# Performance work log

Measured on AMD Instinct MI355X. Metric: run time of the kernel, lower is better.

## Reference

```python
import jax, jax.numpy as jnp
import numpy as np

N_E = 8192      # codebook size
E_DIM = 256     # codebook dim
BETA = 0.25

def setup_inputs() -> dict:
    key = jax.random.key(0)
    k1, k2 = jax.random.split(key)
    z = jax.random.normal(k1, (4, E_DIM, 16, 16, 16), dtype=jnp.float32)
    weight = jax.random.normal(k2, (N_E, E_DIM), dtype=jnp.float32)
    return {"z": z, "weight": weight}

def reference(z, weight):
    # b c d h w -> b d h w c
    z_t = jnp.transpose(z, (0, 2, 3, 4, 1))
    zf = z_t.reshape(-1, E_DIM)                          # [N, e_dim]
    # l2 pairwise distances: |z|^2 + |w|^2 - 2 z.w^T
    d = (jnp.sum(zf * zf, axis=1, keepdims=True)
         + jnp.sum(weight * weight, axis=1)
         - 2.0 * jnp.einsum('bd,nd->bn', zf, weight))    # [N, n_e]
    idx = jnp.argmin(d, axis=1)                          # [N]
    z_q = weight[idx].reshape(z_t.shape)                 # gather lookup
    # perplexity from cluster assignment histogram (avoids dense one-hot)
    counts = jax.ops.segment_sum(jnp.ones_like(idx, dtype=z.dtype), idx,
                                 num_segments=N_E)
    avg_probs = counts / zf.shape[0]
    perplexity = jnp.exp(-jnp.sum(avg_probs * jnp.log(avg_probs + 1e-10)))
    # commitment loss (z_q detached)
    loss = BETA * jnp.mean((jax.lax.stop_gradient(z_q) - z_t) ** 2)
    # straight-through estimator
    z_q_st = z_t + jax.lax.stop_gradient(z_q - z_t)
    out = jnp.transpose(z_q_st, (0, 4, 1, 2, 3))         # b d h w c -> b c d h w
    return out, loss, perplexity, idx
```

## Files before the change

kernel.cpp:

```cpp
#include <hip/hip_runtime.h>
#include <stdint.h>


#define M_TOTAL 16384
#define N_CODES 8192
#define KDIM    256
#define SPATIAL 4096
#define NSPLIT  8
#define CODES_PER_SPLIT  1024
#define CHUNK_CODES      32
#define CHUNKS_PER_SPLIT 32
#define CHUNK_HALFS      8192
#define CHUNK_BYTES      16384

typedef _Float16 v8hf __attribute__((ext_vector_type(8)));
typedef _Float16 v4hf __attribute__((ext_vector_type(4)));
typedef float    v4f  __attribute__((ext_vector_type(4)));

__global__ __launch_bounds__(256) void prep_kernel(
    const float* __restrict__ w, const float* __restrict__ z,
    _Float16* __restrict__ wpk, float* __restrict__ hw_arr,
    _Float16* __restrict__ zfrag,
    int* __restrict__ counts, double* __restrict__ loss_acc,
    int* __restrict__ done_ctr)
{
    const int bid = blockIdx.x;
    const int t = threadIdx.x;
    if (bid < 2048) {
        const int n = bid * 4 + (t >> 6);
        const int lane = t & 63;
        v4f v = ((const v4f*)(w + (size_t)n * KDIM))[lane];
        v4hf hv;
        float s = 0.0f;
#pragma unroll
        for (int j = 0; j < 4; j++) {
            float f = v[j];
            s += f * f;
            hv[j] = (_Float16)f;
        }
        const int chunk = n >> 5;
        const int row   = n & 31;
        const int gg    = (lane >> 1) ^ (n & 7);
        size_t off = (size_t)chunk * CHUNK_HALFS + row * 256 + gg * 8 + (lane & 1) * 4;
        *(v4hf*)(wpk + off) = hv;
#pragma unroll
        for (int o = 32; o >= 1; o >>= 1) s += __shfl_xor(s, o);
        if (lane == 0) hw_arr[n] = 1024.0f - 0.5f * s;
        const int gi = bid * 4 + (t >> 6);
        if (t < 4 && false) {}
        const int ci = bid * 4 + (t & 3);
        if ((t >> 2) == 0) counts[ci] = 0;
        if (bid == 0 && t == 0) { *loss_acc = 0.0; *done_ctr = 0; }
        (void)gi;
    } else {
        const int g16  = (bid - 2048) * 4 + (t >> 6);
        const int lane = t & 63;
        const int r    = lane & 15;
        const int q    = lane >> 4;
        const int row  = g16 * 16 + r;
        const int b    = row >> 12;
        const int s    = row & (SPATIAL - 1);
        const float* zb = z + ((size_t)b << 20) + s;
#pragma unroll
        for (int ks = 0; ks < 8; ks++) {
            v8hf o;
#pragma unroll
            for (int j = 0; j < 8; j++)
                o[j] = (_Float16)zb[(size_t)(ks * 32 + q * 8 + j) << 12];
            *(v8hf*)(zfrag + ((size_t)(g16 * 8 + ks) * 64 + lane) * 8) = o;
        }
    }
}

__device__ __forceinline__ void top2max_merge(uint32_t& v1, int& i1, uint32_t& v2, int& i2,
                                              uint32_t o1, int oi1, uint32_t o2, int oi2) {
    bool ob = (o1 > v1) || (o1 == v1 && oi1 < i1);
    uint32_t n1v, n2v; int n1i, n2i;
    if (ob) {
        bool t2 = (v1 > o2) || (v1 == o2 && i1 < oi2);
        n1v = o1; n1i = oi1;
        n2v = t2 ? v1 : o2; n2i = t2 ? i1 : oi2;
    } else {
        bool t2 = (o1 > v2) || (o1 == v2 && oi1 < i2);
        n1v = v1; n1i = i1;
        n2v = t2 ? o1 : v2; n2i = t2 ? oi1 : i2;
    }
    v1 = n1v; i1 = n1i; v2 = n2v; i2 = n2i;
}

__global__ __launch_bounds__(256, 4) void gemm_kernel(
    const _Float16* __restrict__ zfrag,
    const _Float16* __restrict__ wpk,
    const float* __restrict__ hw_arr,
    int4* __restrict__ candbuf)
{
    __shared__ __align__(16) _Float16 lds[2][CHUNK_HALFS];
    __shared__ float hw_lds[CODES_PER_SPLIT];

    const int bid   = blockIdx.x;
    const int split = bid & 7;
    const int rb    = bid >> 3;
    const int i0    = rb * 128;
    const int tid   = threadIdx.x;
    const int wave  = tid >> 6;
    const int lane  = tid & 63;
    const int r     = lane & 15;
    const int q     = lane >> 4;

    const char* wsplit = (const char*)wpk + (size_t)split * (CODES_PER_SPLIT * KDIM * 2);
    auto stage = [&](int chunk, int buf) {
        const char* gb = wsplit + (size_t)chunk * CHUNK_BYTES + tid * 16;
        _Float16* lb = &lds[buf][tid * 8];
#pragma unroll
        for (int j = 0; j < 4; j++) {
            __builtin_amdgcn_global_load_lds(
                (const __attribute__((address_space(1))) void*)(gb + j * 4096),
                (__attribute__((address_space(3))) void*)(lb + j * 2048), 16, 0, 0);
        }
    };
    stage(0, 0);

    {
        v4f h = *(const v4f*)(hw_arr + split * CODES_PER_SPLIT + tid * 4);
        *(v4f*)&hw_lds[tid * 4] = h;
    }

    v8hf a[2][8];
    {
        const int g16 = (i0 + wave * 32) >> 4;
#pragma unroll
        for (int mt = 0; mt < 2; mt++) {
#pragma unroll
            for (int ks = 0; ks < 8; ks++)
                a[mt][ks] = *(const v8hf*)(zfrag +
                    ((size_t)((g16 + mt) * 8 + ks) * 64 + lane) * 8);
        }
    }

    uint32_t k1[2][4], k2[2][4];
#pragma unroll
    for (int mt = 0; mt < 2; mt++)
#pragma unroll
    for (int g = 0; g < 4; g++) { k1[mt][g] = 0u; k2[mt][g] = 0u; }

    const int swz = r & 7;

    __syncthreads();

#pragma unroll 1
    for (int it = 0; it < CHUNKS_PER_SPLIT; it++) {
        const int buf = it & 1;
        if (it + 1 < CHUNKS_PER_SPLIT) stage(it + 1, buf ^ 1);

        const float hw0 = hw_lds[it * 32 + r];
        const float hw1 = hw_lds[it * 32 + 16 + r];
        v4f acc[2][2];
#pragma unroll
        for (int mt = 0; mt < 2; mt++) {
            acc[mt][0] = (v4f){hw0, hw0, hw0, hw0};
            acc[mt][1] = (v4f){hw1, hw1, hw1, hw1};
        }
        const _Float16* L = &lds[buf][0];
#pragma unroll
        for (int st = 0; st < 2; st++) {
            const int rowoff = (st * 16 + r) * 256;
#pragma unroll
            for (int ks = 0; ks < 8; ks++) {
                const int gran = ((ks << 2) | q) ^ swz;
                v8hf bh = *(const v8hf*)(L + rowoff + (gran << 3));
#pragma unroll
                for (int mt = 0; mt < 2; mt++)
                    acc[mt][st] = __builtin_amdgcn_mfma_f32_16x16x32_f16(a[mt][ks], bh, acc[mt][st], 0, 0, 0);
            }
        }
#pragma unroll
        for (int st = 0; st < 2; st++) {
            const uint32_t tag = (uint32_t)(it * 2 + st);
#pragma unroll
            for (int mt = 0; mt < 2; mt++)
#pragma unroll
            for (int g = 0; g < 4; g++) {
                uint32_t key = (__float_as_uint(acc[mt][st][g]) & 0xFFFFFFC0u) | tag;
                uint32_t o1 = k1[mt][g], o2 = k2[mt][g];
                uint32_t hi = key > o2 ? key : o2;
                k2[mt][g] = hi < o1 ? hi : o1;
                k1[mt][g] = key > o1 ? key : o1;
            }
        }
        __syncthreads();
    }

    const int nsbase = split * CODES_PER_SPLIT + r;
#pragma unroll
    for (int mt = 0; mt < 2; mt++) {
#pragma unroll
        for (int g = 0; g < 4; g++) {
            uint32_t K1 = k1[mt][g], K2 = k2[mt][g];
            int n1 = nsbase + (int)((K1 & 63u) << 4);
            int n2 = nsbase + (int)((K2 & 63u) << 4);
#pragma unroll
            for (int off = 1; off < 16; off <<= 1) {
                uint32_t o1 = __shfl_xor(K1, off);
                int     on1 = __shfl_xor(n1, off);
                uint32_t o2 = __shfl_xor(K2, off);
                int     on2 = __shfl_xor(n2, off);
                top2max_merge(K1, n1, K2, n2, o1, on1, o2, on2);
            }
            if (r == 0) {
                const int row = i0 + wave * 32 + mt * 16 + q * 4 + g;
                candbuf[(size_t)row * 8 + split] = make_int4((int)K1, n1, (int)K2, n2);
            }
        }
    }
}

__global__ __launch_bounds__(256) void finish_kernel(
    const float* __restrict__ z, const float* __restrict__ weight,
    const int4* __restrict__ candbuf,
    int* __restrict__ counts, double* __restrict__ loss_acc,
    int* __restrict__ done_ctr,
    float* __restrict__ out, float* __restrict__ out_scalars,
    float* __restrict__ out_idx_f)
{
    __shared__ int4  s_cand[32][8];
    __shared__ float s_zw[32][KDIM + 1];
    __shared__ int   s_fi[32];
    __shared__ double s_red[4];
    __shared__ int   s_last;

    const int i0 = blockIdx.x * 32;
    const int b  = i0 >> 12;
    const int s0 = i0 & (SPATIAL - 1);
    const int t  = threadIdx.x;

    s_cand[t >> 3][t & 7] = candbuf[(size_t)(i0 + (t >> 3)) * 8 + (t & 7)];

    for (int e = t; e < 32 * KDIM; e += 256) {
        const int c = e >> 5, rr = e & 31;
        s_zw[rr][c] = z[((size_t)b << 20) + ((size_t)c << 12) + s0 + rr];
    }
    __syncthreads();

    const int row = t >> 3, seg = t & 7;
    float zs[32];
#pragma unroll
    for (int j = 0; j < 32; j++) zs[j] = s_zw[row][seg * 32 + j];

    float da[16];
    float dmin_a = 3.4e38f;
#pragma unroll
    for (int sp = 0; sp < 8; sp++) {
        int4 c = s_cand[row][sp];
        da[sp * 2]     = 2048.0f - 2.0f * __uint_as_float((uint32_t)c.x & 0xFFFFFFC0u);
        da[sp * 2 + 1] = 2048.0f - 2.0f * __uint_as_float((uint32_t)c.z & 0xFFFFFFC0u);
        dmin_a = fminf(dmin_a, fminf(da[sp * 2], da[sp * 2 + 1]));
    }
    const float cutoff = dmin_a + 0.5f;

    double dbest = 1e300; int nbest = 0x7fffffff;
#pragma unroll 1
    for (int c = 0; c < 16; c++) {
        if (da[c] > cutoff) continue;
        int4 cc = s_cand[row][c >> 1];
        const int n = (c & 1) ? cc.w : cc.y;
        const float* wr = weight + (size_t)n * KDIM + seg * 32;
        double d = 0.0;
#pragma unroll
        for (int j = 0; j < 32; j++) {
            double df = (double)zs[j] - (double)wr[j];
            d += df * df;
        }
#pragma unroll
        for (int o = 1; o < 8; o <<= 1) d += __shfl_xor(d, o);
        if (d < dbest || (d == dbest && n < nbest)) { dbest = d; nbest = n; }
    }

    double lsum = 0.0;
    if (seg == 0) {
        s_fi[row] = nbest;
        out_idx_f[i0 + row] = (float)nbest;
        atomicAdd(&counts[nbest], 1);
        lsum = dbest;
    }
#pragma unroll
    for (int o = 1; o < 64; o <<= 1) lsum += __shfl_xor(lsum, o);
    if ((t & 63) == 0) s_red[t >> 6] = lsum;
    __syncthreads();
    if (t == 0) atomicAdd(loss_acc, s_red[0] + s_red[1] + s_red[2] + s_red[3]);

    for (int e = t; e < 32 * KDIM; e += 256) {
        const int rr = e >> 8, c = e & 255;
        s_zw[rr][c] = weight[(size_t)s_fi[rr] * KDIM + c];
    }
    __syncthreads();
    const int m = t & 31, c0 = t >> 5;
    const size_t obase = ((size_t)b << 20) + (size_t)(s0 + m);
    for (int c = c0; c < KDIM; c += 8)
        out[obase + ((size_t)c << 12)] = s_zw[m][c];

    if (t == 0) {
        __threadfence();
        int old = __hip_atomic_fetch_add(done_ctr, 1, __ATOMIC_ACQ_REL,
                                         __HIP_MEMORY_SCOPE_AGENT);
        s_last = (old == (int)gridDim.x - 1);
    }
    __syncthreads();
    if (s_last) {
        double s = 0.0;
        for (int n = t; n < N_CODES; n += 256) {
            int c = __hip_atomic_load(&counts[n], __ATOMIC_RELAXED,
                                      __HIP_MEMORY_SCOPE_AGENT);
            double p = (double)c / (double)M_TOTAL;
            s -= p * log(p + 1e-10);
        }
#pragma unroll
        for (int o = 32; o >= 1; o >>= 1) s += __shfl_xor(s, o);
        if ((t & 63) == 0) s_red[t >> 6] = s;
        __syncthreads();
        if (t == 0) {
            double tot = s_red[0] + s_red[1] + s_red[2] + s_red[3];
            double l = __hip_atomic_load(loss_acc, __ATOMIC_RELAXED,
                                         __HIP_MEMORY_SCOPE_AGENT);
            out_scalars[0] = (float)(0.25 * l / (double)(M_TOTAL * KDIM));
            out_scalars[1] = (float)exp(tot);
        }
    }
}

extern "C" void kernel_launch(void* const* d_in, const int* in_sizes, int n_in,
                              void* d_out, int out_size, void* d_ws, size_t ws_size,
                              hipStream_t stream) {
    const float* z      = (const float*)d_in[0];
    const float* weight = (const float*)d_in[1];
    float* out = (float*)d_out;

    size_t off = 0;
    auto carve = [&](size_t bytes) {
        void* p = (char*)d_ws + off;
        off += (bytes + 255) & ~(size_t)255;
        return p;
    };
    _Float16* wpk     = (_Float16*)carve((size_t)N_CODES * KDIM * 2);
    float*    hw_arr  = (float*)   carve((size_t)N_CODES * 4);
    _Float16* zfrag   = (_Float16*)carve((size_t)M_TOTAL * KDIM * 2);
    int4*     candbuf = (int4*)    carve((size_t)M_TOTAL * 8 * 16);
    int*      counts  = (int*)     carve((size_t)N_CODES * 4);
    double*   lossac  = (double*)  carve(16);
    int*      donec   = (int*)     carve(16);

    float* out_scalars = out + (size_t)4 * KDIM * SPATIAL;
    float* out_idx_f   = out_scalars + 2;

    prep_kernel<<<dim3(2048 + 256), dim3(256), 0, stream>>>(
        weight, z, wpk, hw_arr, zfrag, counts, lossac, donec);
    gemm_kernel<<<dim3(128 * NSPLIT), dim3(256), 0, stream>>>(
        zfrag, wpk, hw_arr, candbuf);
    finish_kernel<<<dim3(M_TOTAL / 32), dim3(256), 0, stream>>>(
        z, weight, candbuf, counts, lossac, donec, out, out_scalars, out_idx_f);
}
```

Measured before the change: 219.8 us.

## Fuse prep, GEMM and finish kernels into one persistent kernel with grid barriers

Merges the three launches into a single 1024-block kernel whose phases are separated by software grid barriers (atomic counter plus spin-wait), with the barrier counters cleared by a memset. The z transpose to fp16 fragments now goes through an LDS tile for coalesced writes, and the finish phase handles 16 rows per block instead of 32. This removes two kernel launch gaps and tail effects. The risks are deadlock if all 1024 blocks are not co-resident, an added memset launch, and spin-wait overhead.

```diff
diff --git a/kernel.cpp b/kernel.cpp
--- a/kernel.cpp
+++ b/kernel.cpp
@@ -8,69 +8,14 @@
 #define SPATIAL 4096
 #define NSPLIT  8
 #define CODES_PER_SPLIT  1024
-#define CHUNK_CODES      32
 #define CHUNKS_PER_SPLIT 32
 #define CHUNK_HALFS      8192
 #define CHUNK_BYTES      16384
+#define GRID_BLOCKS      1024
 
 typedef _Float16 v8hf __attribute__((ext_vector_type(8)));
 typedef _Float16 v4hf __attribute__((ext_vector_type(4)));
 typedef float    v4f  __attribute__((ext_vector_type(4)));
-
-__global__ __launch_bounds__(256) void prep_kernel(
-    const float* __restrict__ w, const float* __restrict__ z,
-    _Float16* __restrict__ wpk, float* __restrict__ hw_arr,
-    _Float16* __restrict__ zfrag,
-    int* __restrict__ counts, double* __restrict__ loss_acc,
-    int* __restrict__ done_ctr)
-{
-    const int bid = blockIdx.x;
-    const int t = threadIdx.x;
-    if (bid < 2048) {
-        const int n = bid * 4 + (t >> 6);
-        const int lane = t & 63;
-        v4f v = ((const v4f*)(w + (size_t)n * KDIM))[lane];
-        v4hf hv;
-        float s = 0.0f;
-#pragma unroll
-        for (int j = 0; j < 4; j++) {
-            float f = v[j];
-            s += f * f;
-            hv[j] = (_Float16)f;
-        }
-        const int chunk = n >> 5;
-        const int row   = n & 31;
-        const int gg    = (lane >> 1) ^ (n & 7);
-        size_t off = (size_t)chunk * CHUNK_HALFS + row * 256 + gg * 8 + (lane & 1) * 4;
-        *(v4hf*)(wpk + off) = hv;
-#pragma unroll
-        for (int o = 32; o >= 1; o >>= 1) s += __shfl_xor(s, o);
-        if (lane == 0) hw_arr[n] = 1024.0f - 0.5f * s;
-        const int gi = bid * 4 + (t >> 6);
-        if (t < 4 && false) {}
-        const int ci = bid * 4 + (t & 3);
-        if ((t >> 2) == 0) counts[ci] = 0;
-        if (bid == 0 && t == 0) { *loss_acc = 0.0; *done_ctr = 0; }
-        (void)gi;
-    } else {
-        const int g16  = (bid - 2048) * 4 + (t >> 6);
-        const int lane = t & 63;
-        const int r    = lane & 15;
-        const int q    = lane >> 4;
-        const int row  = g16 * 16 + r;
-        const int b    = row >> 12;
-        const int s    = row & (SPATIAL - 1);
-        const float* zb = z + ((size_t)b << 20) + s;
-#pragma unroll
-        for (int ks = 0; ks < 8; ks++) {
-            v8hf o;
-#pragma unroll
-            for (int j = 0; j < 8; j++)
-                o[j] = (_Float16)zb[(size_t)(ks * 32 + q * 8 + j) << 12];
-            *(v8hf*)(zfrag + ((size_t)(g16 * 8 + ks) * 64 + lane) * 8) = o;
-        }
-    }
-}
 
 __device__ __forceinline__ void top2max_merge(uint32_t& v1, int& i1, uint32_t& v2, int& i2,
                                               uint32_t o1, int oi1, uint32_t o2, int oi2) {
@@ -88,241 +33,309 @@
     v1 = n1v; i1 = n1i; v2 = n2v; i2 = n2i;
 }
 
-__global__ __launch_bounds__(256, 4) void gemm_kernel(
-    const _Float16* __restrict__ zfrag,
-    const _Float16* __restrict__ wpk,
-    const float* __restrict__ hw_arr,
-    int4* __restrict__ candbuf)
-{
-    __shared__ __align__(16) _Float16 lds[2][CHUNK_HALFS];
-    __shared__ float hw_lds[CODES_PER_SPLIT];
-
-    const int bid   = blockIdx.x;
-    const int split = bid & 7;
-    const int rb    = bid >> 3;
-    const int i0    = rb * 128;
-    const int tid   = threadIdx.x;
-    const int wave  = tid >> 6;
-    const int lane  = tid & 63;
-    const int r     = lane & 15;
-    const int q     = lane >> 4;
-
-    const char* wsplit = (const char*)wpk + (size_t)split * (CODES_PER_SPLIT * KDIM * 2);
-    auto stage = [&](int chunk, int buf) {
-        const char* gb = wsplit + (size_t)chunk * CHUNK_BYTES + tid * 16;
-        _Float16* lb = &lds[buf][tid * 8];
-#pragma unroll
-        for (int j = 0; j < 4; j++) {
-            __builtin_amdgcn_global_load_lds(
-                (const __attribute__((address_space(1))) void*)(gb + j * 4096),
-                (__attribute__((address_space(3))) void*)(lb + j * 2048), 16, 0, 0);
-        }
-    };
-    stage(0, 0);
-
-    {
-        v4f h = *(const v4f*)(hw_arr + split * CODES_PER_SPLIT + tid * 4);
-        *(v4f*)&hw_lds[tid * 4] = h;
-    }
-
-    v8hf a[2][8];
-    {
-        const int g16 = (i0 + wave * 32) >> 4;
-#pragma unroll
-        for (int mt = 0; mt < 2; mt++) {
-#pragma unroll
-            for (int ks = 0; ks < 8; ks++)
-                a[mt][ks] = *(const v8hf*)(zfrag +
-                    ((size_t)((g16 + mt) * 8 + ks) * 64 + lane) * 8);
-        }
-    }
-
-    uint32_t k1[2][4], k2[2][4];
-#pragma unroll
-    for (int mt = 0; mt < 2; mt++)
-#pragma unroll
-    for (int g = 0; g < 4; g++) { k1[mt][g] = 0u; k2[mt][g] = 0u; }
-
-    const int swz = r & 7;
-
+__device__ __forceinline__ void grid_barrier(int* sem) {
     __syncthreads();
-
-#pragma unroll 1
-    for (int it = 0; it < CHUNKS_PER_SPLIT; it++) {
-        const int buf = it & 1;
-        if (it + 1 < CHUNKS_PER_SPLIT) stage(it + 1, buf ^ 1);
-
-        const float hw0 = hw_lds[it * 32 + r];
-        const float hw1 = hw_lds[it * 32 + 16 + r];
-        v4f acc[2][2];
-#pragma unroll
-        for (int mt = 0; mt < 2; mt++) {
-            acc[mt][0] = (v4f){hw0, hw0, hw0, hw0};
-            acc[mt][1] = (v4f){hw1, hw1, hw1, hw1};
-        }
-        const _Float16* L = &lds[buf][0];
-#pragma unroll
-        for (int st = 0; st < 2; st++) {
-            const int rowoff = (st * 16 + r) * 256;
-#pragma unroll
-            for (int ks = 0; ks < 8; ks++) {
-                const int gran = ((ks << 2) | q) ^ swz;
-                v8hf bh = *(const v8hf*)(L + rowoff + (gran << 3));
-#pragma unroll
-                for (int mt = 0; mt < 2; mt++)
-                    acc[mt][st] = __builtin_amdgcn_mfma_f32_16x16x32_f16(a[mt][ks], bh, acc[mt][st], 0, 0, 0);
-            }
-        }
-#pragma unroll
-        for (int st = 0; st < 2; st++) {
-            const uint32_t tag = (uint32_t)(it * 2 + st);
-#pragma unroll
-            for (int mt = 0; mt < 2; mt++)
-#pragma unroll
-            for (int g = 0; g < 4; g++) {
-                uint32_t key = (__float_as_uint(acc[mt][st][g]) & 0xFFFFFFC0u) | tag;
-                uint32_t o1 = k1[mt][g], o2 = k2[mt][g];
-                uint32_t hi = key > o2 ? key : o2;
-                k2[mt][g] = hi < o1 ? hi : o1;
-                k1[mt][g] = key > o1 ? key : o1;
-            }
-        }
-        __syncthreads();
-    }
-
-    const int nsbase = split * CODES_PER_SPLIT + r;
-#pragma unroll
-    for (int mt = 0; mt < 2; mt++) {
-#pragma unroll
-        for (int g = 0; g < 4; g++) {
-            uint32_t K1 = k1[mt][g], K2 = k2[mt][g];
-            int n1 = nsbase + (int)((K1 & 63u) << 4);
-            int n2 = nsbase + (int)((K2 & 63u) << 4);
-#pragma unroll
-            for (int off = 1; off < 16; off <<= 1) {
-                uint32_t o1 = __shfl_xor(K1, off);
-                int     on1 = __shfl_xor(n1, off);
-                uint32_t o2 = __shfl_xor(K2, off);
-                int     on2 = __shfl_xor(n2, off);
-                top2max_merge(K1, n1, K2, n2, o1, on1, o2, on2);
-            }
-            if (r == 0) {
-                const int row = i0 + wave * 32 + mt * 16 + q * 4 + g;
-                candbuf[(size_t)row * 8 + split] = make_int4((int)K1, n1, (int)K2, n2);
-            }
-        }
-    }
+    if (threadIdx.x == 0) {
+        __threadfence();
+        __hip_atomic_fetch_add(sem, 1, __ATOMIC_ACQ_REL, __HIP_MEMORY_SCOPE_AGENT);
+        while (__hip_atomic_load(sem, __ATOMIC_ACQUIRE, __HIP_MEMORY_SCOPE_AGENT)
+               < GRID_BLOCKS) {
+            __builtin_amdgcn_s_sleep(2);
+        }
+    }
+    __syncthreads();
 }
 
-__global__ __launch_bounds__(256) void finish_kernel(
-    const float* __restrict__ z, const float* __restrict__ weight,
-    const int4* __restrict__ candbuf,
+__global__ __launch_bounds__(256, 4) void vq_fused_kernel(
+    const float* __restrict__ z, const float* __restrict__ w,
+    _Float16* __restrict__ wpk, float* __restrict__ hw_arr,
+    _Float16* __restrict__ zfrag, int4* __restrict__ candbuf,
     int* __restrict__ counts, double* __restrict__ loss_acc,
-    int* __restrict__ done_ctr,
+    int* __restrict__ ctrl,
     float* __restrict__ out, float* __restrict__ out_scalars,
     float* __restrict__ out_idx_f)
 {
-    __shared__ int4  s_cand[32][8];
-    __shared__ float s_zw[32][KDIM + 1];
-    __shared__ int   s_fi[32];
-    __shared__ double s_red[4];
-    __shared__ int   s_last;
-
-    const int i0 = blockIdx.x * 32;
-    const int b  = i0 >> 12;
-    const int s0 = i0 & (SPATIAL - 1);
-    const int t  = threadIdx.x;
-
-    s_cand[t >> 3][t & 7] = candbuf[(size_t)(i0 + (t >> 3)) * 8 + (t & 7)];
-
-    for (int e = t; e < 32 * KDIM; e += 256) {
-        const int c = e >> 5, rr = e & 31;
-        s_zw[rr][c] = z[((size_t)b << 20) + ((size_t)c << 12) + s0 + rr];
-    }
-    __syncthreads();
-
-    const int row = t >> 3, seg = t & 7;
-    float zs[32];
-#pragma unroll
-    for (int j = 0; j < 32; j++) zs[j] = s_zw[row][seg * 32 + j];
-
-    float da[16];
-    float dmin_a = 3.4e38f;
-#pragma unroll
-    for (int sp = 0; sp < 8; sp++) {
-        int4 c = s_cand[row][sp];
-        da[sp * 2]     = 2048.0f - 2.0f * __uint_as_float((uint32_t)c.x & 0xFFFFFFC0u);
-        da[sp * 2 + 1] = 2048.0f - 2.0f * __uint_as_float((uint32_t)c.z & 0xFFFFFFC0u);
-        dmin_a = fminf(dmin_a, fminf(da[sp * 2], da[sp * 2 + 1]));
-    }
-    const float cutoff = dmin_a + 0.5f;
-
-    double dbest = 1e300; int nbest = 0x7fffffff;
+    __shared__ __align__(16) char smem[36864];
+
+    const int bid = blockIdx.x;
+    const int tid = threadIdx.x;
+    const int wave = tid >> 6;
+    const int lane = tid & 63;
+
+    {
+        _Float16 (*tile)[18] = (_Float16 (*)[18])smem;
+        const int i0z = bid * 16;
+        const int bz  = i0z >> 12;
+        const int s0z = i0z & (SPATIAL - 1);
+        const float* zb = z + ((size_t)bz << 20) + s0z;
+#pragma unroll
+        for (int i = 0; i < 16; i++) {
+            const int e = i * 256 + tid;
+            const int k = e >> 4, rr = e & 15;
+            tile[k][rr] = (_Float16)zb[((size_t)k << 12) + rr];
+        }
+
+#pragma unroll
+        for (int rep = 0; rep < 2; rep++) {
+            const int n = bid * 8 + wave * 2 + rep;
+            v4f v = ((const v4f*)(w + (size_t)n * KDIM))[lane];
+            v4hf hv;
+            float s = 0.0f;
+#pragma unroll
+            for (int j = 0; j < 4; j++) {
+                float f = v[j];
+                s += f * f;
+                hv[j] = (_Float16)f;
+            }
+            const int chunk = n >> 5;
+            const int row   = n & 31;
+            const int gg    = (lane >> 1) ^ (n & 7);
+            size_t off = (size_t)chunk * CHUNK_HALFS + row * 256 + gg * 8 + (lane & 1) * 4;
+            *(v4hf*)(wpk + off) = hv;
+#pragma unroll
+            for (int o = 32; o >= 1; o >>= 1) s += __shfl_xor(s, o);
+            if (lane == 0) hw_arr[n] = 1024.0f - 0.5f * s;
+        }
+        if (tid < 8) counts[bid * 8 + tid] = 0;
+        if (bid == 0 && tid == 0) *loss_acc = 0.0;
+
+        __syncthreads();
+#pragma unroll
+        for (int rep = 0; rep < 2; rep++) {
+            const int sidx = rep * 256 + tid;
+            const int ks = sidx >> 6, l2 = sidx & 63;
+            const int r2 = l2 & 15, q2 = l2 >> 4;
+            v8hf o;
+#pragma unroll
+            for (int j = 0; j < 8; j++)
+                o[j] = tile[ks * 32 + q2 * 8 + j][r2];
+            *(v8hf*)(zfrag + ((size_t)(bid * 8 + ks) * 64 + l2) * 8) = o;
+        }
+    }
+
+    grid_barrier(&ctrl[0]);
+
+    {
+        _Float16* lds = (_Float16*)smem;
+        float* hw_lds = (float*)(smem + 32768);
+
+        const int split = bid & 7;
+        const int rb    = bid >> 3;
+        const int i0    = rb * 128;
+        const int r     = lane & 15;
+        const int q     = lane >> 4;
+
+        const char* wsplit = (const char*)wpk + (size_t)split * (CODES_PER_SPLIT * KDIM * 2);
+        auto stage = [&](int chunk, int buf) {
+            const char* gb = wsplit + (size_t)chunk * CHUNK_BYTES + tid * 16;
+            _Float16* lb = lds + buf * CHUNK_HALFS + tid * 8;
+#pragma unroll
+            for (int j = 0; j < 4; j++) {
+                __builtin_amdgcn_global_load_lds(
+                    (const __attribute__((address_space(1))) void*)(gb + j * 4096),
+                    (__attribute__((address_space(3))) void*)(lb + j * 2048), 16, 0, 0);
+            }
+        };
+        stage(0, 0);
+
+        {
+            v4f h = *(const v4f*)(hw_arr + split * CODES_PER_SPLIT + tid * 4);
+            *(v4f*)&hw_lds[tid * 4] = h;
+        }
+
+        v8hf a[2][8];
+        {
+            const int g16 = (i0 + wave * 32) >> 4;
+#pragma unroll
+            for (int mt = 0; mt < 2; mt++) {
+#pragma unroll
+                for (int ks = 0; ks < 8; ks++)
+                    a[mt][ks] = *(const v8hf*)(zfrag +
+                        ((size_t)((g16 + mt) * 8 + ks) * 64 + lane) * 8);
+            }
+        }
+
+        uint32_t k1[2][4], k2[2][4];
+#pragma unroll
+        for (int mt = 0; mt < 2; mt++)
+#pragma unroll
+        for (int g = 0; g < 4; g++) { k1[mt][g] = 0u; k2[mt][g] = 0u; }
+
+        const int swz = r & 7;
+        __syncthreads();
+
 #pragma unroll 1
-    for (int c = 0; c < 16; c++) {
-        if (da[c] > cutoff) continue;
-        int4 cc = s_cand[row][c >> 1];
-        const int n = (c & 1) ? cc.w : cc.y;
-        const float* wr = weight + (size_t)n * KDIM + seg * 32;
-        double d = 0.0;
-#pragma unroll
-        for (int j = 0; j < 32; j++) {
-            double df = (double)zs[j] - (double)wr[j];
-            d += df * df;
-        }
-#pragma unroll
-        for (int o = 1; o < 8; o <<= 1) d += __shfl_xor(d, o);
-        if (d < dbest || (d == dbest && n < nbest)) { dbest = d; nbest = n; }
-    }
-
-    double lsum = 0.0;
-    if (seg == 0) {
-        s_fi[row] = nbest;
-        out_idx_f[i0 + row] = (float)nbest;
-        atomicAdd(&counts[nbest], 1);
-        lsum = dbest;
-    }
-#pragma unroll
-    for (int o = 1; o < 64; o <<= 1) lsum += __shfl_xor(lsum, o);
-    if ((t & 63) == 0) s_red[t >> 6] = lsum;
-    __syncthreads();
-    if (t == 0) atomicAdd(loss_acc, s_red[0] + s_red[1] + s_red[2] + s_red[3]);
-
-    for (int e = t; e < 32 * KDIM; e += 256) {
-        const int rr = e >> 8, c = e & 255;
-        s_zw[rr][c] = weight[(size_t)s_fi[rr] * KDIM + c];
-    }
-    __syncthreads();
-    const int m = t & 31, c0 = t >> 5;
-    const size_t obase = ((size_t)b << 20) + (size_t)(s0 + m);
-    for (int c = c0; c < KDIM; c += 8)
-        out[obase + ((size_t)c << 12)] = s_zw[m][c];
-
-    if (t == 0) {
-        __threadfence();
-        int old = __hip_atomic_fetch_add(done_ctr, 1, __ATOMIC_ACQ_REL,
-                                         __HIP_MEMORY_SCOPE_AGENT);
-        s_last = (old == (int)gridDim.x - 1);
-    }
-    __syncthreads();
-    if (s_last) {
-        double s = 0.0;
-        for (int n = t; n < N_CODES; n += 256) {
-            int c = __hip_atomic_load(&counts[n], __ATOMIC_RELAXED,
-                                      __HIP_MEMORY_SCOPE_AGENT);
-            double p = (double)c / (double)M_TOTAL;
-            s -= p * log(p + 1e-10);
-        }
-#pragma unroll
-        for (int o = 32; o >= 1; o >>= 1) s += __shfl_xor(s, o);
-        if ((t & 63) == 0) s_red[t >> 6] = s;
-        __syncthreads();
+        for (int it = 0; it < CHUNKS_PER_SPLIT; it++) {
+            const int buf = it & 1;
+            if (it + 1 < CHUNKS_PER_SPLIT) stage(it + 1, buf ^ 1);
+
+            const float hw0 = hw_lds[it * 32 + r];
+            const float hw1 = hw_lds[it * 32 + 16 + r];
+            v4f acc[2][2];
+#pragma unroll
+            for (int mt = 0; mt < 2; mt++) {
+                acc[mt][0] = (v4f){hw0, hw0, hw0, hw0};
+                acc[mt][1] = (v4f){hw1, hw1, hw1, hw1};
+            }
+            const _Float16* L = lds + buf * CHUNK_HALFS;
+#pragma unroll
+            for (int st = 0; st < 2; st++) {
+                const int rowoff = (st * 16 + r) * 256;
+#pragma unroll
+                for (int ks = 0; ks < 8; ks++) {
+                    const int gran = ((ks << 2) | q) ^ swz;
+                    v8hf bh = *(const v8hf*)(L + rowoff + (gran << 3));
+#pragma unroll
+                    for (int mt = 0; mt < 2; mt++)
+                        acc[mt][st] = __builtin_amdgcn_mfma_f32_16x16x32_f16(a[mt][ks], bh, acc[mt][st], 0, 0, 0);
+                }
+            }
+#pragma unroll
+            for (int st = 0; st < 2; st++) {
+                const uint32_t tag = (uint32_t)(it * 2 + st);
+#pragma unroll
+                for (int mt = 0; mt < 2; mt++)
+#pragma unroll
+                for (int g = 0; g < 4; g++) {
+                    uint32_t key = (__float_as_uint(acc[mt][st][g]) & 0xFFFFFFC0u) | tag;
+                    uint32_t o1 = k1[mt][g], o2 = k2[mt][g];
+                    uint32_t hi = key > o2 ? key : o2;
+                    k2[mt][g] = hi < o1 ? hi : o1;
+                    k1[mt][g] = key > o1 ? key : o1;
+                }
+            }
+            __syncthreads();
+        }
+
+        const int nsbase = split * CODES_PER_SPLIT + r;
+#pragma unroll
+        for (int mt = 0; mt < 2; mt++) {
+#pragma unroll
+            for (int g = 0; g < 4; g++) {
+                uint32_t K1 = k1[mt][g], K2 = k2[mt][g];
+                int n1 = nsbase + (int)((K1 & 63u) << 4);
+                int n2 = nsbase + (int)((K2 & 63u) << 4);
+#pragma unroll
+                for (int off = 1; off < 16; off <<= 1) {
+                    uint32_t o1 = __shfl_xor(K1, off);
+                    int     on1 = __shfl_xor(n1, off);
+                    uint32_t o2 = __shfl_xor(K2, off);
+                    int     on2 = __shfl_xor(n2, off);
+                    top2max_merge(K1, n1, K2, n2, o1, on1, o2, on2);
+                }
+                if (r == 0) {
+                    const int row = i0 + wave * 32 + mt * 16 + q * 4 + g;
+                    candbuf[(size_t)row * 8 + split] = make_int4((int)K1, n1, (int)K2, n2);
+                }
+            }
+        }
+    }
+
+    grid_barrier(&ctrl[1]);
+
+    {
+        int4 (*s_cand)[8] = (int4 (*)[8])smem;
+        float (*s_zw)[257] = (float (*)[257])(smem + 2048);
+        int*    s_fi  = (int*)(smem + 2048 + 16448);
+        double* s_red = (double*)(smem + 2048 + 16448 + 64);
+        int*    s_last = (int*)(smem + 2048 + 16448 + 64 + 32);
+
+        const int i0 = bid * 16;
+        const int b  = i0 >> 12;
+        const int s0 = i0 & (SPATIAL - 1);
+        const int t  = tid;
+
+        if (t < 128) s_cand[t >> 3][t & 7] = candbuf[(size_t)(i0 + (t >> 3)) * 8 + (t & 7)];
+
+        for (int e = t; e < 16 * KDIM; e += 256) {
+            const int c = e >> 4, rr = e & 15;
+            s_zw[rr][c] = z[((size_t)b << 20) + ((size_t)c << 12) + s0 + rr];
+        }
+        __syncthreads();
+
+        const int row = t >> 4, seg = t & 15;
+        float zs[16];
+#pragma unroll
+        for (int j = 0; j < 16; j++) zs[j] = s_zw[row][seg * 16 + j];
+
+        float da[16];
+        float dmin_a = 3.4e38f;
+#pragma unroll
+        for (int sp = 0; sp < 8; sp++) {
+            int4 c = s_cand[row][sp];
+            da[sp * 2]     = 2048.0f - 2.0f * __uint_as_float((uint32_t)c.x & 0xFFFFFFC0u);
+            da[sp * 2 + 1] = 2048.0f - 2.0f * __uint_as_float((uint32_t)c.z & 0xFFFFFFC0u);
+            dmin_a = fminf(dmin_a, fminf(da[sp * 2], da[sp * 2 + 1]));
+        }
+        const float cutoff = dmin_a + 0.5f;
+
+        double dbest = 1e300; int nbest = 0x7fffffff;
+#pragma unroll 1
+        for (int c = 0; c < 16; c++) {
+            if (da[c] > cutoff) continue;
+            int4 cc = s_cand[row][c >> 1];
+            const int n = (c & 1) ? cc.w : cc.y;
+            const float* wr = w + (size_t)n * KDIM + seg * 16;
+            double d = 0.0;
+#pragma unroll
+            for (int j = 0; j < 16; j++) {
+                double df = (double)zs[j] - (double)wr[j];
+                d += df * df;
+            }
+#pragma unroll
+            for (int o = 1; o < 16; o <<= 1) d += __shfl_xor(d, o);
+            if (d < dbest || (d == dbest && n < nbest)) { dbest = d; nbest = n; }
+        }
+
+        double lsum = 0.0;
+        if (seg == 0) {
+            s_fi[row] = nbest;
+            out_idx_f[i0 + row] = (float)nbest;
+            atomicAdd(&counts[nbest], 1);
+            lsum = dbest;
+        }
+#pragma unroll
+        for (int o = 1; o < 64; o <<= 1) lsum += __shfl_xor(lsum, o);
+        if ((t & 63) == 0) s_red[t >> 6] = lsum;
+        __syncthreads();
+        if (t == 0) atomicAdd(loss_acc, s_red[0] + s_red[1] + s_red[2] + s_red[3]);
+
+        for (int e = t; e < 16 * KDIM; e += 256) {
+            const int rr = e >> 8, c = e & 255;
+            s_zw[rr][c] = w[(size_t)s_fi[rr] * KDIM + c];
+        }
+        __syncthreads();
+        const int m = t & 15, c0 = t >> 4;
+        const size_t obase = ((size_t)b << 20) + (size_t)(s0 + m);
+        for (int c = c0; c < KDIM; c += 16)
+            out[obase + ((size_t)c << 12)] = s_zw[m][c];
+
         if (t == 0) {
-            double tot = s_red[0] + s_red[1] + s_red[2] + s_red[3];
-            double l = __hip_atomic_load(loss_acc, __ATOMIC_RELAXED,
-                                         __HIP_MEMORY_SCOPE_AGENT);
-            out_scalars[0] = (float)(0.25 * l / (double)(M_TOTAL * KDIM));
-            out_scalars[1] = (float)exp(tot);
+            __threadfence();
+            int old = __hip_atomic_fetch_add(&ctrl[2], 1, __ATOMIC_ACQ_REL,
+                                             __HIP_MEMORY_SCOPE_AGENT);
+            *s_last = (old == GRID_BLOCKS - 1);
+        }
+        __syncthreads();
+        if (*s_last) {
+            double s = 0.0;
+            for (int n = t; n < N_CODES; n += 256) {
+                int c = __hip_atomic_load(&counts[n], __ATOMIC_RELAXED,
+                                          __HIP_MEMORY_SCOPE_AGENT);
+                double p = (double)c / (double)M_TOTAL;
+                s -= p * log(p + 1e-10);
+            }
+#pragma unroll
+            for (int o = 32; o >= 1; o >>= 1) s += __shfl_xor(s, o);
+            if ((t & 63) == 0) s_red[t >> 6] = s;
+            __syncthreads();
+            if (t == 0) {
+                double tot = s_red[0] + s_red[1] + s_red[2] + s_red[3];
+                double l = __hip_atomic_load(loss_acc, __ATOMIC_RELAXED,
+                                             __HIP_MEMORY_SCOPE_AGENT);
+                out_scalars[0] = (float)(0.25 * l / (double)(M_TOTAL * KDIM));
+                out_scalars[1] = (float)exp(tot);
+            }
         }
     }
 }
@@ -346,15 +359,13 @@
     int4*     candbuf = (int4*)    carve((size_t)M_TOTAL * 8 * 16);
     int*      counts  = (int*)     carve((size_t)N_CODES * 4);
     double*   lossac  = (double*)  carve(16);
-    int*      donec   = (int*)     carve(16);
+    int*      ctrl    = (int*)     carve(256);
 
     float* out_scalars = out + (size_t)4 * KDIM * SPATIAL;
     float* out_idx_f   = out_scalars + 2;
 
-    prep_kernel<<<dim3(2048 + 256), dim3(256), 0, stream>>>(
-        weight, z, wpk, hw_arr, zfrag, counts, lossac, donec);
-    gemm_kernel<<<dim3(128 * NSPLIT), dim3(256), 0, stream>>>(
-        zfrag, wpk, hw_arr, candbuf);
-    finish_kernel<<<dim3(M_TOTAL / 32), dim3(256), 0, stream>>>(
-        z, weight, candbuf, counts, lossac, donec, out, out_scalars, out_idx_f);
+    (void)hipMemsetAsync(ctrl, 0, 256, stream);
+    vq_fused_kernel<<<dim3(GRID_BLOCKS), dim3(256), 0, stream>>>(
+        z, weight, wpk, hw_arr, zfrag, candbuf, counts, lossac, ctrl,
+        out, out_scalars, out_idx_f);
 }
```

Result: slower. 566.1 us (+157.5%).
